# Optimization experiments

Hardware: AMD Instinct MI355X
Metric: run time of the kernel (lower is better)

The kernel has to match this reference:

```python
import jax, jax.numpy as jnp
import numpy as np

DIM = 1024
NUM_HEADS = 8  # only used for the scale; heads are never actually split
SCALE = float((DIM // NUM_HEADS) ** 0.5)


def _attn(x, wq, wk, wv):
    # Single-head full-dim attention, faithful to the source (no head split).
    Q = x @ wq.T  # [B,S,D]
    K = x @ wk.T
    V = x @ wv.T
    scores = jnp.einsum('bqd,bkd->bqk', Q, K) / SCALE  # [B,S,S]
    attn = jax.nn.softmax(scores, axis=-1)
    return jnp.einsum('bqk,bkd->bqd', attn, V)


def setup_inputs() -> dict:
    key = jax.random.key(0)
    ks = jax.random.split(key, 9)
    B, S, D = 4, 2048, DIM
    w = lambda k: jax.random.normal(k, (D, D), dtype=jnp.float32) * 0.02
    return {
        'x': jax.random.normal(ks[0], (B, S, D), dtype=jnp.float32),
        'wq1': w(ks[1]), 'wk1': w(ks[2]), 'wv1': w(ks[3]),
        'fc1_w': w(ks[4]),
        'wq2': w(ks[5]), 'wk2': w(ks[6]), 'wv2': w(ks[7]),
        'fc2_w': w(ks[8]),
    }


def reference(x, wq1, wk1, wv1, fc1_w, wq2, wk2, wv2, fc2_w):
    h = _attn(x, wq1, wk1, wv1)
    h = jax.nn.silu(h)
    h = h @ fc1_w.T
    h = _attn(h, wq2, wk2, wv2)
    h = jax.nn.silu(h)
    h = h @ fc2_w.T
    return jax.nn.softmax(h, axis=-1)
```

## Files before the change

### kernel.cpp

```cpp
#include <hip/hip_runtime.h>
#include <math.h>


typedef __attribute__((ext_vector_type(8))) int i32x8;
typedef __attribute__((ext_vector_type(4))) int i32x4;
typedef __attribute__((ext_vector_type(4))) float f32x4;
typedef unsigned char u8;
typedef unsigned int u32;

#define EPI_F8 1
#define EPI_RV 2
#define EPI_EXP 3
#define EPI_PV 4
#define EPI_EXPF32 5

__device__ __forceinline__ void gload_lds16(const void* g, void* l) {
    __builtin_amdgcn_global_load_lds(
        (const __attribute__((address_space(1))) void*)g,
        (__attribute__((address_space(3))) void*)l, 16, 0, 0);
}

__device__ __forceinline__ u8 cvt_f8(float v) {
    return (u8)(__builtin_amdgcn_cvt_pk_fp8_f32(v, v, 0, false) & 0xFF);
}

__device__ __forceinline__ u32 pack_f8x4(float v0, float v1, float v2, float v3) {
    int p01 = __builtin_amdgcn_cvt_pk_fp8_f32(v0, v1, 0, false);
    int p23 = __builtin_amdgcn_cvt_pk_fp8_f32(v2, v3, 0, false);
    return (u32)(p01 & 0xFFFF) | ((u32)p23 << 16);
}

template <int EPI>
__global__ __launch_bounds__(256) void gemm_fp8(
    const u8* __restrict__ A, const u8* __restrict__ B,
    void* __restrict__ C0, void* __restrict__ C1, void* __restrict__ C2,
    int K, int ldA, int ldB, int ldC,
    long long bsA, long long bsB, long long bsC, float alpha, float beta)
{
    __shared__ u8 sA[128 * 128];
    __shared__ u8 sB[128 * 128];

    const int tid = threadIdx.x;
    const int wave = tid >> 6, lane = tid & 63;
    const int wm = wave >> 1, wn = wave & 1;
    const int m0 = blockIdx.y * 128, n0 = blockIdx.x * 128;
    const long long z = blockIdx.z;

    const u8* pA = A + z * bsA;
    const u8* pB = B + z * bsB;

    int blkid[4], rs_[4], cs16[4];
#pragma unroll
    for (int i = 0; i < 4; i++) {
        blkid[i] = wave * 256 + i * 64 + lane;
        rs_[i] = blkid[i] >> 3;
        cs16[i] = ((blkid[i] & 7) ^ (rs_[i] & 7)) * 16;
    }

    f32x4 acc[4][4] = {};
    const int fr = lane & 15, fc2 = (lane >> 4) * 2;

    for (int k0 = 0; k0 < K; k0 += 128) {
#pragma unroll
        for (int i = 0; i < 4; i++) {
            gload_lds16(pA + (long long)(m0 + rs_[i]) * ldA + k0 + cs16[i],
                        sA + blkid[i] * 16);
            gload_lds16(pB + (long long)(n0 + rs_[i]) * ldB + k0 + cs16[i],
                        sB + blkid[i] * 16);
        }
        __syncthreads();

        i32x8 a[4], b[4];
#pragma unroll
        for (int i = 0; i < 4; i++) {
            const int row = wm * 64 + i * 16 + fr;
            const int sw = row & 7;
            i32x4 lo = *(const i32x4*)(sA + row * 128 + ((fc2 + 0) ^ sw) * 16);
            i32x4 hi = *(const i32x4*)(sA + row * 128 + ((fc2 + 1) ^ sw) * 16);
            a[i] = __builtin_shufflevector(lo, hi, 0, 1, 2, 3, 4, 5, 6, 7);
        }
#pragma unroll
        for (int j = 0; j < 4; j++) {
            const int row = wn * 64 + j * 16 + fr;
            const int sw = row & 7;
            i32x4 lo = *(const i32x4*)(sB + row * 128 + ((fc2 + 0) ^ sw) * 16);
            i32x4 hi = *(const i32x4*)(sB + row * 128 + ((fc2 + 1) ^ sw) * 16);
            b[j] = __builtin_shufflevector(lo, hi, 0, 1, 2, 3, 4, 5, 6, 7);
        }
#pragma unroll
        for (int i = 0; i < 4; i++)
#pragma unroll
            for (int j = 0; j < 4; j++)
                acc[i][j] = __builtin_amdgcn_mfma_scale_f32_16x16x128_f8f6f4(
                    a[i], b[j], acc[i][j], 0 , 0 ,
                    0, 0x7F7F7F7F, 0, 0x7F7F7F7F);
        __syncthreads();
    }

    const int col = lane & 15;
    const int rbase = (lane >> 4) * 4;

    if (EPI == EPI_F8) {
#pragma unroll
        for (int j = 0; j < 4; j++) {
            const int Cq = n0 + wn * 64 + j * 16 + col;
#pragma unroll
            for (int i = 0; i < 4; i++) {
                const int R0 = m0 + wm * 64 + i * 16 + rbase;
                u8* C = (u8*)C0 + z * bsC;
                *(u32*)(C + (long long)Cq * ldC + R0) =
                    pack_f8x4(acc[i][j][0] * alpha, acc[i][j][1] * alpha,
                              acc[i][j][2] * alpha, acc[i][j][3] * alpha);
            }
        }
    }
    (void)beta; (void)C1; (void)C2;
}

template <int EPI>
__global__ __launch_bounds__(512, 2) void gemm256(
    const u8* __restrict__ A, const u8* __restrict__ B,
    void* __restrict__ C0, void* __restrict__ C1, void* __restrict__ C2,
    int K, int ldA, int ldB, int ldC,
    long long bsA, long long bsB, long long bsC, float alpha, float beta)
{
    __shared__ __align__(16) u8 sA[3][128 * 128];
    __shared__ __align__(16) u8 sB[3][256 * 128];

    const int tid = threadIdx.x;
    const int wave = tid >> 6, lane = tid & 63;
    const int wm = wave >> 2, wn = wave & 3;
    const int m0 = blockIdx.y * 128, n0 = blockIdx.x * 256;
    const long long z = blockIdx.z;

    const u8* pA = A + z * bsA;
    const u8* pB = B + z * bsB;

    long long offA[2], offB[4];
    int dstA[2], dstB[4];
#pragma unroll
    for (int l = 0; l < 2; l++) {
        const int id = l * 512 + tid;
        const int r = id >> 3, c = (id & 7) ^ (r & 7);
        offA[l] = (long long)(m0 + r) * ldA + c * 16;
        dstA[l] = id * 16;
    }
#pragma unroll
    for (int l = 0; l < 4; l++) {
        const int id = l * 512 + tid;
        const int r = id >> 3, c = (id & 7) ^ (r & 7);
        offB[l] = (long long)(n0 + r) * ldB + c * 16;
        dstB[l] = id * 16;
    }

    f32x4 acc[4][4] = {};
    const int fr = lane & 15, fc2 = (lane >> 4) * 2;
    const int NT = K >> 7;

    auto STAGE = [&](int t, int buf) {
        const long long kb = (long long)t << 7;
#pragma unroll
        for (int l = 0; l < 2; l++)
            gload_lds16(pA + offA[l] + kb, &sA[buf][dstA[l]]);
#pragma unroll
        for (int l = 0; l < 4; l++)
            gload_lds16(pB + offB[l] + kb, &sB[buf][dstB[l]]);
    };

    auto COMPUTE = [&](int buf) {
        i32x8 a[4], b[4];
#pragma unroll
        for (int i = 0; i < 4; i++) {
            const int row = wm * 64 + i * 16 + fr;
            const int sw = row & 7;
            const u8* p = &sA[buf][row * 128];
            i32x4 lo = *(const i32x4*)(p + ((fc2 + 0) ^ sw) * 16);
            i32x4 hi = *(const i32x4*)(p + ((fc2 + 1) ^ sw) * 16);
            a[i] = __builtin_shufflevector(lo, hi, 0, 1, 2, 3, 4, 5, 6, 7);
        }
#pragma unroll
        for (int j = 0; j < 4; j++) {
            const int row = wn * 64 + j * 16 + fr;
            const int sw = row & 7;
            const u8* p = &sB[buf][row * 128];
            i32x4 lo = *(const i32x4*)(p + ((fc2 + 0) ^ sw) * 16);
            i32x4 hi = *(const i32x4*)(p + ((fc2 + 1) ^ sw) * 16);
            b[j] = __builtin_shufflevector(lo, hi, 0, 1, 2, 3, 4, 5, 6, 7);
        }
        __builtin_amdgcn_s_setprio(1);
#pragma unroll
        for (int i = 0; i < 4; i++)
#pragma unroll
            for (int j = 0; j < 4; j++)
                acc[i][j] = __builtin_amdgcn_mfma_scale_f32_16x16x128_f8f6f4(
                    a[i], b[j], acc[i][j], 0 , 0 ,
                    0, 0x7F7F7F7F, 0, 0x7F7F7F7F);
        __builtin_amdgcn_s_setprio(0);
    };

    STAGE(0, 0);
    STAGE(1, 1);
    asm volatile("s_waitcnt vmcnt(6)" ::: "memory");
    __builtin_amdgcn_s_barrier();
    __builtin_amdgcn_sched_barrier(0);

    int c0 = 0, c1 = 1, c2 = 2;
    for (int t = 0; t < NT - 2; ++t) {
        STAGE(t + 2, c2);
        COMPUTE(c0);
        asm volatile("s_waitcnt vmcnt(6) lgkmcnt(0)" ::: "memory");
        __builtin_amdgcn_s_barrier();
        __builtin_amdgcn_sched_barrier(0);
        const int tmp = c0; c0 = c1; c1 = c2; c2 = tmp;
    }
    COMPUTE(c0);
    asm volatile("s_waitcnt vmcnt(0) lgkmcnt(0)" ::: "memory");
    __builtin_amdgcn_s_barrier();
    __builtin_amdgcn_sched_barrier(0);
    COMPUTE(c1);

    const int col = lane & 15;
    const int rbase = (lane >> 4) * 4;

    if (EPI == EPI_EXP) {
        u8* P = (u8*)C0 + z * bsC;
        float* rsum = (float*)C1 + z * 2048;
#pragma unroll
        for (int j = 0; j < 4; j++) {
            const int Cq = n0 + wn * 64 + j * 16 + col;
            float part = 0.f;
#pragma unroll
            for (int i = 0; i < 4; i++) {
                const int R0 = m0 + wm * 64 + i * 16 + rbase;
                float e0 = __expf(acc[i][j][0] * alpha);
                float e1 = __expf(acc[i][j][1] * alpha);
                float e2 = __expf(acc[i][j][2] * alpha);
                float e3 = __expf(acc[i][j][3] * alpha);
                part += (e0 + e1) + (e2 + e3);
                *(u32*)(P + (long long)Cq * ldC + R0) =
                    pack_f8x4(e0 * 0.0625f, e1 * 0.0625f,
                              e2 * 0.0625f, e3 * 0.0625f);
            }
            part += __shfl_xor(part, 16);
            part += __shfl_xor(part, 32);
            if (lane < 16) atomicAdd(&rsum[Cq], part);
        }
        return;
    }

    if (EPI == EPI_EXPF32) {
        float* Cw = (float*)C0;
        float* rsum = (float*)C1;
#pragma unroll
        for (int j = 0; j < 4; j++) {
            const int Cq = n0 + wn * 64 + j * 16 + col;
            float part = 0.f;
#pragma unroll
            for (int i = 0; i < 4; i++) {
                const int R0 = m0 + wm * 64 + i * 16 + rbase;
                float4 e;
                e.x = __expf(acc[i][j][0] * alpha);
                e.y = __expf(acc[i][j][1] * alpha);
                e.z = __expf(acc[i][j][2] * alpha);
                e.w = __expf(acc[i][j][3] * alpha);
                part += (e.x + e.y) + (e.z + e.w);
                *(float4*)(Cw + (long long)Cq * ldC + R0) = e;
            }
            part += __shfl_xor(part, 16);
            part += __shfl_xor(part, 32);
            if (lane < 16) atomicAdd(&rsum[Cq], part);
        }
        return;
    }

#pragma unroll
    for (int j = 0; j < 4; j++) {
        const int Cq = n0 + wn * 64 + j * 16 + col;
        float inv;
        if (EPI == EPI_PV) {
            const float* rsum = (const float*)C1 + z * 2048;
            inv = alpha / rsum[Cq];
        }
#pragma unroll
        for (int i = 0; i < 4; i++) {
            const int R0 = m0 + wm * 64 + i * 16 + rbase;
            if (EPI == EPI_F8) {
                u8* C = (u8*)C0 + z * bsC;
                *(u32*)(C + (long long)Cq * ldC + R0) =
                    pack_f8x4(acc[i][j][0] * alpha, acc[i][j][1] * alpha,
                              acc[i][j][2] * alpha, acc[i][j][3] * alpha);
            } else if (EPI == EPI_PV) {
                u8* C = (u8*)C0 + z * bsC;
                float v[4];
#pragma unroll
                for (int r = 0; r < 4; r++) {
                    float t = acc[i][j][r] * inv;
                    v[r] = (t / (1.f + __expf(-t))) * beta;
                }
                *(u32*)(C + (long long)Cq * ldC + R0) =
                    pack_f8x4(v[0], v[1], v[2], v[3]);
            } else {
                const int seg = R0 >> 10;
                const int db = R0 & 1023;
                if (seg == 1) {
                    const int bb = Cq >> 11, tt = Cq & 2047;
                    u8* VTp = (u8*)C2;
#pragma unroll
                    for (int r = 0; r < 4; r++)
                        VTp[(long long)bb * (1024LL * 2048) +
                            (long long)(db + r) * 2048 + tt] =
                            cvt_f8(acc[i][j][r] * beta);
                } else {
                    u8* C = (u8*)C0;
                    *(u32*)(C + (long long)Cq * 1024 + db) =
                        pack_f8x4(acc[i][j][0] * alpha, acc[i][j][1] * alpha,
                                  acc[i][j][2] * alpha, acc[i][j][3] * alpha);
                }
            }
        }
    }
}

__global__ __launch_bounds__(256) void convert_all(
    const float* x, const float* wv1, const float* wv2, const float* fc1,
    const float* fc2, u8* __restrict__ ax, u8* __restrict__ bproj,
    u8* __restrict__ wfc, float* __restrict__ rz)
{
    const int bid = blockIdx.x;
    if (bid < 24) {
        float4 zero = {0.f, 0.f, 0.f, 0.f};
        *(float4*)(rz + ((long long)bid * 256 + threadIdx.x) * 4) = zero;
    }
    const float* src;
    u8* dst;
    float scale;
    long long i;
    if (bid < 8192) {
        src = x; dst = ax; scale = 8.f;
        i = ((long long)bid * 256 + threadIdx.x) * 4;
    } else {
        const int idx = bid - 8192;
        const int wi = idx >> 10;
        const float* srcs[4] = {wv1, wv2, fc1, fc2};
        u8* dsts[4] = {bproj + (1 << 20), bproj + 3 * (1 << 20),
                       wfc, wfc + (1 << 20)};
        src = srcs[wi]; dst = dsts[wi]; scale = 256.f;
        i = (((long long)(idx & 1023)) * 256 + threadIdx.x) * 4;
    }
    float4 v = *(const float4*)(src + i);
    *(u32*)(dst + i) = pack_f8x4(v.x * scale, v.y * scale,
                                 v.z * scale, v.w * scale);
}

__global__ __launch_bounds__(256) void convert_t(
    const float* wq1, const float* wk1, const float* wq2, const float* wk2,
    u8* __restrict__ o)
{
    const float* srcs[4] = {wq1, wk1, wq2, wk2};
    const float* src = srcs[blockIdx.y];
    u8* dst = o + (long long)blockIdx.y * (1 << 20);
    const int q0 = (blockIdx.x & 15) * 64, d0 = (blockIdx.x >> 4) * 64;
    const int qq = (threadIdx.x & 15) * 4, dd = (threadIdx.x >> 4) * 4;
    float4 v[4];
#pragma unroll
    for (int s = 0; s < 4; s++)
        v[s] = *(const float4*)(src + (long long)(q0 + qq + s) * 1024 + d0 + dd);
    const float* vf = (const float*)v;
#pragma unroll
    for (int r = 0; r < 4; r++)
        *(u32*)(dst + (long long)(d0 + dd + r) * 1024 + q0 + qq) =
            pack_f8x4(vf[0 * 4 + r] * 256.f, vf[1 * 4 + r] * 256.f,
                      vf[2 * 4 + r] * 256.f, vf[3 * 4 + r] * 256.f);
}

__global__ __launch_bounds__(256) void normalize_1024(
    const float* __restrict__ e, const float* __restrict__ rsum,
    float* __restrict__ out)
{
    const long long row = blockIdx.x;
    const float inv = 1.0f / rsum[row];
    const float* p = e + row * 1024;
    float* o = out + row * 1024;
    float4 v = *(const float4*)(p + threadIdx.x * 4);
    float4 ov;
    ov.x = v.x * inv; ov.y = v.y * inv; ov.z = v.z * inv; ov.w = v.w * inv;
    *(float4*)(o + threadIdx.x * 4) = ov;
}

extern "C" void kernel_launch(void* const* d_in, const int* in_sizes, int n_in,
                              void* d_out, int out_size, void* d_ws, size_t ws_size,
                              hipStream_t stream)
{
    float* out = (float*)d_out;

    constexpr int Bt = 4, S = 2048, D = 1024;
    constexpr int M = Bt * S;
    const long long MD = (long long)M * D;
    const long long DD = (long long)D * D;
    const long long SD = (long long)S * D;
    const long long SS = (long long)S * S;

    u8* Af = (u8*)d_ws;
    u8* Bproj = Af + MD;
    u8* WqT = Bproj + 2 * 2048 * 1024;
    u8* Wfc = WqT + 4 * DD;
    u8* Rf = Wfc + 2 * DD;
    u8* VT = Rf + MD;
    u8* Pf = VT + MD;
    u8* Hs = Pf + (long long)Bt * SS;
    float* SC = (float*)(Hs + MD);
    float* rsum0 = SC + MD;
    float* rsum1 = rsum0 + M;
    float* rsum2 = rsum1 + M;

    const dim3 blk(256);
    const dim3 blk2(512);

    const float SOFT = 0.08838834764831845f;
    const float a_d1   = 1.f / 64.f;
    const float a_R[2] = {1.f / 512.f, 1.f / 1024.f};
    const float b_V[2] = {1.f / 256.f, 1.f / 64.f};
    const float a_qk[2] = {SOFT / 128.f, SOFT / 65536.f};
    const float a_pv[2] = {2.0f, 1.f / 64.f};
    const float b_pv[2] = {256.f, 65536.f};
    const float a_fc[2] = {256.f / 65536.f, 1.f / 16777216.f};

    convert_all<<<dim3(12288), blk, 0, stream>>>(
        (const float*)d_in[0], (const float*)d_in[3], (const float*)d_in[7],
        (const float*)d_in[4], (const float*)d_in[8], Af, Bproj, Wfc, rsum0);
    convert_t<<<dim3(256, 4), blk, 0, stream>>>(
        (const float*)d_in[1], (const float*)d_in[2], (const float*)d_in[5],
        (const float*)d_in[6], WqT);
    gemm_fp8<EPI_F8><<<dim3(8, 8, 2), blk, 0, stream>>>(
        WqT, WqT + DD, Bproj, nullptr, nullptr, D, D, D, D,
        2 * DD, 2 * DD, (long long)2048 * 1024, a_d1, 0.f);

    const dim3 grv(M / 256, 2048 / 128, 1);
    const dim3 gqk(S / 256, S / 128, Bt);
    const dim3 gpv(S / 256, D / 128, Bt);
    const dim3 gw(M / 256, D / 128, 1);

    for (int layer = 0; layer < 2; layer++) {
        const u8* bp = Bproj + (long long)layer * 2048 * 1024;
        const u8* fc = Wfc + (long long)layer * DD;
        float* rsum = layer ? rsum1 : rsum0;

        gemm256<EPI_RV><<<grv, blk2, 0, stream>>>(
            bp, Af, Rf, nullptr, VT, D, D, D, D, 0, 0, 0,
            a_R[layer], b_V[layer]);
        gemm256<EPI_EXP><<<gqk, blk2, 0, stream>>>(
            Af, Rf, Pf, rsum, nullptr, D, D, D, S, SD, SD, SS,
            a_qk[layer], 0.f);
        gemm256<EPI_PV><<<gpv, blk2, 0, stream>>>(
            VT, Pf, Hs, rsum, nullptr, S, S, S, D,
            (long long)D * S, SS, SD, a_pv[layer], b_pv[layer]);
        if (layer == 0) {
            gemm256<EPI_F8><<<gw, blk2, 0, stream>>>(
                fc, Hs, Af, nullptr, nullptr, D, D, D, D, 0, 0, 0,
                a_fc[0], 0.f);
        } else {
            gemm256<EPI_EXPF32><<<gw, blk2, 0, stream>>>(
                fc, Hs, SC, rsum2, nullptr, D, D, D, D, 0, 0, 0,
                a_fc[1], 0.f);
        }
    }

    normalize_1024<<<dim3(M), blk, 0, stream>>>(SC, rsum2, out);
}
```

Measured before the change: 357.4 us.

## Restructure gemm256 into a two-buffer, four-phase interleaved load/MFMA schedule

The triple-buffered gemm256 main loop is replaced with a double-buffered loop. Each K-step is split into four quadrant phases. Each phase reads only the A/B fragments it needs from LDS, issues part of the next tiles' global-to-LDS loads, and runs four MFMAs under raised priority, with barriers between phases. The goal is to spread LDS reads and global loads across the MFMA work and to cut shared memory use. The cost is many more barriers per iteration and less prefetch depth.

```diff
diff --git a/kernel.cpp b/kernel.cpp
--- a/kernel.cpp
+++ b/kernel.cpp
@@ -29,6 +29,10 @@
     int p23 = __builtin_amdgcn_cvt_pk_fp8_f32(v2, v3, 0, false);
     return (u32)(p01 & 0xFFFF) | ((u32)p23 << 16);
 }
+
+#define MFMA_F8(a, b, c) \
+    __builtin_amdgcn_mfma_scale_f32_16x16x128_f8f6f4( \
+        (a), (b), (c), 0, 0, 0, 0x7F7F7F7F, 0, 0x7F7F7F7F)
 
 template <int EPI>
 __global__ __launch_bounds__(256) void gemm_fp8(
@@ -91,9 +95,7 @@
         for (int i = 0; i < 4; i++)
 #pragma unroll
             for (int j = 0; j < 4; j++)
-                acc[i][j] = __builtin_amdgcn_mfma_scale_f32_16x16x128_f8f6f4(
-                    a[i], b[j], acc[i][j], 0 , 0 ,
-                    0, 0x7F7F7F7F, 0, 0x7F7F7F7F);
+                acc[i][j] = MFMA_F8(a[i], b[j], acc[i][j]);
         __syncthreads();
     }
 
@@ -124,8 +126,8 @@
     int K, int ldA, int ldB, int ldC,
     long long bsA, long long bsB, long long bsC, float alpha, float beta)
 {
-    __shared__ __align__(16) u8 sA[3][128 * 128];
-    __shared__ __align__(16) u8 sB[3][256 * 128];
+    __shared__ __align__(16) u8 sA[2][128 * 128];
+    __shared__ __align__(16) u8 sB[2][256 * 128];
 
     const int tid = threadIdx.x;
     const int wave = tid >> 6, lane = tid & 63;
@@ -157,67 +159,101 @@
     const int fr = lane & 15, fc2 = (lane >> 4) * 2;
     const int NT = K >> 7;
 
-    auto STAGE = [&](int t, int buf) {
+    auto SA = [&](int t) {
         const long long kb = (long long)t << 7;
+        u8* base = sA[t & 1];
 #pragma unroll
         for (int l = 0; l < 2; l++)
-            gload_lds16(pA + offA[l] + kb, &sA[buf][dstA[l]]);
-#pragma unroll
-        for (int l = 0; l < 4; l++)
-            gload_lds16(pB + offB[l] + kb, &sB[buf][dstB[l]]);
+            gload_lds16(pA + offA[l] + kb, base + dstA[l]);
     };
-
-    auto COMPUTE = [&](int buf) {
-        i32x8 a[4], b[4];
-#pragma unroll
-        for (int i = 0; i < 4; i++) {
-            const int row = wm * 64 + i * 16 + fr;
-            const int sw = row & 7;
-            const u8* p = &sA[buf][row * 128];
-            i32x4 lo = *(const i32x4*)(p + ((fc2 + 0) ^ sw) * 16);
-            i32x4 hi = *(const i32x4*)(p + ((fc2 + 1) ^ sw) * 16);
-            a[i] = __builtin_shufflevector(lo, hi, 0, 1, 2, 3, 4, 5, 6, 7);
-        }
-#pragma unroll
-        for (int j = 0; j < 4; j++) {
-            const int row = wn * 64 + j * 16 + fr;
-            const int sw = row & 7;
-            const u8* p = &sB[buf][row * 128];
-            i32x4 lo = *(const i32x4*)(p + ((fc2 + 0) ^ sw) * 16);
-            i32x4 hi = *(const i32x4*)(p + ((fc2 + 1) ^ sw) * 16);
-            b[j] = __builtin_shufflevector(lo, hi, 0, 1, 2, 3, 4, 5, 6, 7);
-        }
+    auto SB = [&](int t, int h) {
+        const long long kb = (long long)t << 7;
+        u8* base = sB[t & 1];
+#pragma unroll
+        for (int l = 2 * h; l < 2 * h + 2; l++)
+            gload_lds16(pB + offB[l] + kb, base + dstB[l]);
+    };
+
+    auto RDA = [&](int buf, int i) -> i32x8 {
+        const int row = wm * 64 + i * 16 + fr;
+        const int sw = row & 7;
+        const u8* p = &sA[buf][row * 128];
+        i32x4 lo = *(const i32x4*)(p + ((fc2 + 0) ^ sw) * 16);
+        i32x4 hi = *(const i32x4*)(p + ((fc2 + 1) ^ sw) * 16);
+        return __builtin_shufflevector(lo, hi, 0, 1, 2, 3, 4, 5, 6, 7);
+    };
+    auto RDB = [&](int buf, int j) -> i32x8 {
+        const int row = wn * 64 + j * 16 + fr;
+        const int sw = row & 7;
+        const u8* p = &sB[buf][row * 128];
+        i32x4 lo = *(const i32x4*)(p + ((fc2 + 0) ^ sw) * 16);
+        i32x4 hi = *(const i32x4*)(p + ((fc2 + 1) ^ sw) * 16);
+        return __builtin_shufflevector(lo, hi, 0, 1, 2, 3, 4, 5, 6, 7);
+    };
+
+    SA(0); SB(0, 0); SB(0, 1); SB(1, 0); SB(1, 1);
+    asm volatile("s_waitcnt vmcnt(4)" ::: "memory");
+    __builtin_amdgcn_sched_barrier(0);
+    __builtin_amdgcn_s_barrier();
+
+    for (int t = 0; t < NT; ++t) {
+        const int buf = t & 1;
+        i32x8 a0, a1, a2, a3, b0, b1, b2, b3;
+
+        a0 = RDA(buf, 0); a1 = RDA(buf, 1);
+        b0 = RDB(buf, 0); b1 = RDB(buf, 1);
+        if (t + 1 < NT) SA(t + 1);
+        __builtin_amdgcn_s_barrier();
+        asm volatile("s_waitcnt lgkmcnt(0)" ::: "memory");
+        __builtin_amdgcn_sched_barrier(0);
         __builtin_amdgcn_s_setprio(1);
-#pragma unroll
-        for (int i = 0; i < 4; i++)
-#pragma unroll
-            for (int j = 0; j < 4; j++)
-                acc[i][j] = __builtin_amdgcn_mfma_scale_f32_16x16x128_f8f6f4(
-                    a[i], b[j], acc[i][j], 0 , 0 ,
-                    0, 0x7F7F7F7F, 0, 0x7F7F7F7F);
+        acc[0][0] = MFMA_F8(a0, b0, acc[0][0]);
+        acc[0][1] = MFMA_F8(a0, b1, acc[0][1]);
+        acc[1][0] = MFMA_F8(a1, b0, acc[1][0]);
+        acc[1][1] = MFMA_F8(a1, b1, acc[1][1]);
         __builtin_amdgcn_s_setprio(0);
-    };
-
-    STAGE(0, 0);
-    STAGE(1, 1);
-    asm volatile("s_waitcnt vmcnt(6)" ::: "memory");
-    __builtin_amdgcn_s_barrier();
-    __builtin_amdgcn_sched_barrier(0);
-
-    int c0 = 0, c1 = 1, c2 = 2;
-    for (int t = 0; t < NT - 2; ++t) {
-        STAGE(t + 2, c2);
-        COMPUTE(c0);
-        asm volatile("s_waitcnt vmcnt(6) lgkmcnt(0)" ::: "memory");
-        __builtin_amdgcn_s_barrier();
+        __builtin_amdgcn_s_barrier();
+
+        b2 = RDB(buf, 2); b3 = RDB(buf, 3);
+        __builtin_amdgcn_s_barrier();
+        asm volatile("s_waitcnt lgkmcnt(0)" ::: "memory");
         __builtin_amdgcn_sched_barrier(0);
-        const int tmp = c0; c0 = c1; c1 = c2; c2 = tmp;
-    }
-    COMPUTE(c0);
-    asm volatile("s_waitcnt vmcnt(0) lgkmcnt(0)" ::: "memory");
-    __builtin_amdgcn_s_barrier();
-    __builtin_amdgcn_sched_barrier(0);
-    COMPUTE(c1);
+        __builtin_amdgcn_s_setprio(1);
+        acc[0][2] = MFMA_F8(a0, b2, acc[0][2]);
+        acc[0][3] = MFMA_F8(a0, b3, acc[0][3]);
+        acc[1][2] = MFMA_F8(a1, b2, acc[1][2]);
+        acc[1][3] = MFMA_F8(a1, b3, acc[1][3]);
+        __builtin_amdgcn_s_setprio(0);
+        __builtin_amdgcn_s_barrier();
+
+        a2 = RDA(buf, 2); a3 = RDA(buf, 3);
+        if (t + 2 < NT) SB(t + 2, 0);
+        __builtin_amdgcn_s_barrier();
+        asm volatile("s_waitcnt lgkmcnt(0)" ::: "memory");
+        __builtin_amdgcn_sched_barrier(0);
+        __builtin_amdgcn_s_setprio(1);
+        acc[2][0] = MFMA_F8(a2, b0, acc[2][0]);
+        acc[2][1] = MFMA_F8(a2, b1, acc[2][1]);
+        acc[3][0] = MFMA_F8(a3, b0, acc[3][0]);
+        acc[3][1] = MFMA_F8(a3, b1, acc[3][1]);
+        __builtin_amdgcn_s_setprio(0);
+        __builtin_amdgcn_s_barrier();
+
+        if (t + 2 < NT) SB(t + 2, 1);
+        __builtin_amdgcn_s_barrier();
+        __builtin_amdgcn_s_setprio(1);
+        acc[2][2] = MFMA_F8(a2, b2, acc[2][2]);
+        acc[2][3] = MFMA_F8(a2, b3, acc[2][3]);
+        acc[3][2] = MFMA_F8(a3, b2, acc[3][2]);
+        acc[3][3] = MFMA_F8(a3, b3, acc[3][3]);
+        __builtin_amdgcn_s_setprio(0);
+        if (t + 2 < NT)
+            asm volatile("s_waitcnt vmcnt(4)" ::: "memory");
+        else
+            asm volatile("s_waitcnt vmcnt(0)" ::: "memory");
+        __builtin_amdgcn_sched_barrier(0);
+        __builtin_amdgcn_s_barrier();
+    }
 
     const int col = lane & 15;
     const int rbase = (lane >> 4) * 4;
```

After: 357.6 us. No clear change (+0.0%).

## Replace 128x256 triple-buffered GEMM with 64x256 double-buffered tile kernel

Applied to the files above, without the earlier changes.

The main fp8 GEMM drops its block tile from 128x256 to 64x256. Each of the 8 waves now computes a 64x32 slice instead of a 64x64 quadrant, and the 3-stage pipeline with manual waitcnt and barriers becomes a simple 2-stage double buffer using __syncthreads. Launch bounds move to 4 blocks per CU and grids double in the M dimension. This aims at more occupancy and less LDS per block, but it halves MFMA work per loaded B tile, lowers arithmetic intensity, and drops the priority and scheduling hints.

```diff
diff --git a/kernel.cpp b/kernel.cpp
--- a/kernel.cpp
+++ b/kernel.cpp
@@ -29,6 +29,10 @@
     int p23 = __builtin_amdgcn_cvt_pk_fp8_f32(v2, v3, 0, false);
     return (u32)(p01 & 0xFFFF) | ((u32)p23 << 16);
 }
+
+#define MFMA_F8(a, b, c) \
+    __builtin_amdgcn_mfma_scale_f32_16x16x128_f8f6f4( \
+        (a), (b), (c), 0, 0, 0, 0x7F7F7F7F, 0, 0x7F7F7F7F)
 
 template <int EPI>
 __global__ __launch_bounds__(256) void gemm_fp8(
@@ -91,9 +95,7 @@
         for (int i = 0; i < 4; i++)
 #pragma unroll
             for (int j = 0; j < 4; j++)
-                acc[i][j] = __builtin_amdgcn_mfma_scale_f32_16x16x128_f8f6f4(
-                    a[i], b[j], acc[i][j], 0 , 0 ,
-                    0, 0x7F7F7F7F, 0, 0x7F7F7F7F);
+                acc[i][j] = MFMA_F8(a[i], b[j], acc[i][j]);
         __syncthreads();
     }
 
@@ -118,33 +120,29 @@
 }
 
 template <int EPI>
-__global__ __launch_bounds__(512, 2) void gemm256(
+__global__ __launch_bounds__(512, 4) void gemm64(
     const u8* __restrict__ A, const u8* __restrict__ B,
     void* __restrict__ C0, void* __restrict__ C1, void* __restrict__ C2,
     int K, int ldA, int ldB, int ldC,
     long long bsA, long long bsB, long long bsC, float alpha, float beta)
 {
-    __shared__ __align__(16) u8 sA[3][128 * 128];
-    __shared__ __align__(16) u8 sB[3][256 * 128];
+    __shared__ __align__(16) u8 sA[2][64 * 128];
+    __shared__ __align__(16) u8 sB[2][256 * 128];
 
     const int tid = threadIdx.x;
     const int wave = tid >> 6, lane = tid & 63;
-    const int wm = wave >> 2, wn = wave & 3;
-    const int m0 = blockIdx.y * 128, n0 = blockIdx.x * 256;
+    const int m0 = blockIdx.y * 64, n0 = blockIdx.x * 256;
     const long long z = blockIdx.z;
 
     const u8* pA = A + z * bsA;
     const u8* pB = B + z * bsB;
 
-    long long offA[2], offB[4];
-    int dstA[2], dstB[4];
-#pragma unroll
-    for (int l = 0; l < 2; l++) {
-        const int id = l * 512 + tid;
-        const int r = id >> 3, c = (id & 7) ^ (r & 7);
-        offA[l] = (long long)(m0 + r) * ldA + c * 16;
-        dstA[l] = id * 16;
-    }
+    const int rA = tid >> 3;
+    const long long offA = (long long)(m0 + rA) * ldA +
+                           (((tid & 7) ^ (rA & 7)) * 16);
+    const int dstA = tid * 16;
+    long long offB[4];
+    int dstB[4];
 #pragma unroll
     for (int l = 0; l < 4; l++) {
         const int id = l * 512 + tid;
@@ -153,25 +151,30 @@
         dstB[l] = id * 16;
     }
 
-    f32x4 acc[4][4] = {};
+    f32x4 acc[4][2] = {};
     const int fr = lane & 15, fc2 = (lane >> 4) * 2;
     const int NT = K >> 7;
 
-    auto STAGE = [&](int t, int buf) {
+    auto STAGE = [&](int t) {
         const long long kb = (long long)t << 7;
-#pragma unroll
-        for (int l = 0; l < 2; l++)
-            gload_lds16(pA + offA[l] + kb, &sA[buf][dstA[l]]);
+        const int buf = t & 1;
+        gload_lds16(pA + offA + kb, &sA[buf][dstA]);
 #pragma unroll
         for (int l = 0; l < 4; l++)
             gload_lds16(pB + offB[l] + kb, &sB[buf][dstB[l]]);
     };
 
-    auto COMPUTE = [&](int buf) {
-        i32x8 a[4], b[4];
+    STAGE(0);
+    __syncthreads();
+
+    for (int t = 0; t < NT; ++t) {
+        if (t + 1 < NT) STAGE(t + 1);
+
+        const int buf = t & 1;
+        i32x8 a[4], b[2];
 #pragma unroll
         for (int i = 0; i < 4; i++) {
-            const int row = wm * 64 + i * 16 + fr;
+            const int row = i * 16 + fr;
             const int sw = row & 7;
             const u8* p = &sA[buf][row * 128];
             i32x4 lo = *(const i32x4*)(p + ((fc2 + 0) ^ sw) * 16);
@@ -179,45 +182,22 @@
             a[i] = __builtin_shufflevector(lo, hi, 0, 1, 2, 3, 4, 5, 6, 7);
         }
 #pragma unroll
-        for (int j = 0; j < 4; j++) {
-            const int row = wn * 64 + j * 16 + fr;
+        for (int j = 0; j < 2; j++) {
+            const int row = wave * 32 + j * 16 + fr;
             const int sw = row & 7;
             const u8* p = &sB[buf][row * 128];
             i32x4 lo = *(const i32x4*)(p + ((fc2 + 0) ^ sw) * 16);
             i32x4 hi = *(const i32x4*)(p + ((fc2 + 1) ^ sw) * 16);
             b[j] = __builtin_shufflevector(lo, hi, 0, 1, 2, 3, 4, 5, 6, 7);
         }
-        __builtin_amdgcn_s_setprio(1);
 #pragma unroll
         for (int i = 0; i < 4; i++)
 #pragma unroll
-            for (int j = 0; j < 4; j++)
-                acc[i][j] = __builtin_amdgcn_mfma_scale_f32_16x16x128_f8f6f4(
-                    a[i], b[j], acc[i][j], 0 , 0 ,
-                    0, 0x7F7F7F7F, 0, 0x7F7F7F7F);
-        __builtin_amdgcn_s_setprio(0);
-    };
-
-    STAGE(0, 0);
-    STAGE(1, 1);
-    asm volatile("s_waitcnt vmcnt(6)" ::: "memory");
-    __builtin_amdgcn_s_barrier();
-    __builtin_amdgcn_sched_barrier(0);
-
-    int c0 = 0, c1 = 1, c2 = 2;
-    for (int t = 0; t < NT - 2; ++t) {
-        STAGE(t + 2, c2);
-        COMPUTE(c0);
-        asm volatile("s_waitcnt vmcnt(6) lgkmcnt(0)" ::: "memory");
-        __builtin_amdgcn_s_barrier();
-        __builtin_amdgcn_sched_barrier(0);
-        const int tmp = c0; c0 = c1; c1 = c2; c2 = tmp;
-    }
-    COMPUTE(c0);
-    asm volatile("s_waitcnt vmcnt(0) lgkmcnt(0)" ::: "memory");
-    __builtin_amdgcn_s_barrier();
-    __builtin_amdgcn_sched_barrier(0);
-    COMPUTE(c1);
+            for (int j = 0; j < 2; j++)
+                acc[i][j] = MFMA_F8(a[i], b[j], acc[i][j]);
+
+        __syncthreads();
+    }
 
     const int col = lane & 15;
     const int rbase = (lane >> 4) * 4;
@@ -226,12 +206,12 @@
         u8* P = (u8*)C0 + z * bsC;
         float* rsum = (float*)C1 + z * 2048;
 #pragma unroll
-        for (int j = 0; j < 4; j++) {
-            const int Cq = n0 + wn * 64 + j * 16 + col;
+        for (int j = 0; j < 2; j++) {
+            const int Cq = n0 + wave * 32 + j * 16 + col;
             float part = 0.f;
 #pragma unroll
             for (int i = 0; i < 4; i++) {
-                const int R0 = m0 + wm * 64 + i * 16 + rbase;
+                const int R0 = m0 + i * 16 + rbase;
                 float e0 = __expf(acc[i][j][0] * alpha);
                 float e1 = __expf(acc[i][j][1] * alpha);
                 float e2 = __expf(acc[i][j][2] * alpha);
@@ -252,12 +232,12 @@
         float* Cw = (float*)C0;
         float* rsum = (float*)C1;
 #pragma unroll
-        for (int j = 0; j < 4; j++) {
-            const int Cq = n0 + wn * 64 + j * 16 + col;
+        for (int j = 0; j < 2; j++) {
+            const int Cq = n0 + wave * 32 + j * 16 + col;
             float part = 0.f;
 #pragma unroll
             for (int i = 0; i < 4; i++) {
-                const int R0 = m0 + wm * 64 + i * 16 + rbase;
+                const int R0 = m0 + i * 16 + rbase;
                 float4 e;
                 e.x = __expf(acc[i][j][0] * alpha);
                 e.y = __expf(acc[i][j][1] * alpha);
@@ -274,8 +254,8 @@
     }
 
 #pragma unroll
-    for (int j = 0; j < 4; j++) {
-        const int Cq = n0 + wn * 64 + j * 16 + col;
+    for (int j = 0; j < 2; j++) {
+        const int Cq = n0 + wave * 32 + j * 16 + col;
         float inv;
         if (EPI == EPI_PV) {
             const float* rsum = (const float*)C1 + z * 2048;
@@ -283,7 +263,7 @@
         }
 #pragma unroll
         for (int i = 0; i < 4; i++) {
-            const int R0 = m0 + wm * 64 + i * 16 + rbase;
+            const int R0 = m0 + i * 16 + rbase;
             if (EPI == EPI_F8) {
                 u8* C = (u8*)C0 + z * bsC;
                 *(u32*)(C + (long long)Cq * ldC + R0) =
@@ -435,31 +415,31 @@
         WqT, WqT + DD, Bproj, nullptr, nullptr, D, D, D, D,
         2 * DD, 2 * DD, (long long)2048 * 1024, a_d1, 0.f);
 
-    const dim3 grv(M / 256, 2048 / 128, 1);
-    const dim3 gqk(S / 256, S / 128, Bt);
-    const dim3 gpv(S / 256, D / 128, Bt);
-    const dim3 gw(M / 256, D / 128, 1);
+    const dim3 grv(M / 256, 2048 / 64, 1);
+    const dim3 gqk(S / 256, S / 64, Bt);
+    const dim3 gpv(S / 256, D / 64, Bt);
+    const dim3 gw(M / 256, D / 64, 1);
 
     for (int layer = 0; layer < 2; layer++) {
         const u8* bp = Bproj + (long long)layer * 2048 * 1024;
         const u8* fc = Wfc + (long long)layer * DD;
         float* rsum = layer ? rsum1 : rsum0;
 
-        gemm256<EPI_RV><<<grv, blk2, 0, stream>>>(
+        gemm64<EPI_RV><<<grv, blk2, 0, stream>>>(
             bp, Af, Rf, nullptr, VT, D, D, D, D, 0, 0, 0,
             a_R[layer], b_V[layer]);
-        gemm256<EPI_EXP><<<gqk, blk2, 0, stream>>>(
+        gemm64<EPI_EXP><<<gqk, blk2, 0, stream>>>(
             Af, Rf, Pf, rsum, nullptr, D, D, D, S, SD, SD, SS,
             a_qk[layer], 0.f);
-        gemm256<EPI_PV><<<gpv, blk2, 0, stream>>>(
+        gemm64<EPI_PV><<<gpv, blk2, 0, stream>>>(
             VT, Pf, Hs, rsum, nullptr, S, S, S, D,
             (long long)D * S, SS, SD, a_pv[layer], b_pv[layer]);
         if (layer == 0) {
-            gemm256<EPI_F8><<<gw, blk2, 0, stream>>>(
+            gemm64<EPI_F8><<<gw, blk2, 0, stream>>>(
                 fc, Hs, Af, nullptr, nullptr, D, D, D, D, 0, 0, 0,
                 a_fc[0], 0.f);
         } else {
-            gemm256<EPI_EXPF32><<<gw, blk2, 0, stream>>>(
+            gemm64<EPI_EXPF32><<<gw, blk2, 0, stream>>>(
                 fc, Hs, SC, rsum2, nullptr, D, D, D, D, 0, 0, 0,
                 a_fc[1], 0.f);
         }
```

After: 341.8 us. -4.4%, faster.

## Replace triple-buffered GEMM pipeline with single-buffered synchronous main loop

Applied to the files above, without the earlier changes.

Removes the three-stage LDS ring buffer, manual vmcnt waits, sched barriers and priority hints from the 256-wide FP8 GEMM. Each K step now loads one tile, syncs, computes, and syncs again. LDS use drops from 144KB to 48KB per block and the launch-bounds occupancy hint is gone, which may let more blocks share a CU. In exchange, global loads no longer overlap with MFMA work, so latency is exposed on every iteration.

```diff
diff --git a/kernel.cpp b/kernel.cpp
--- a/kernel.cpp
+++ b/kernel.cpp
@@ -29,6 +29,10 @@
     int p23 = __builtin_amdgcn_cvt_pk_fp8_f32(v2, v3, 0, false);
     return (u32)(p01 & 0xFFFF) | ((u32)p23 << 16);
 }
+
+#define MFMA_F8(a, b, c) \
+    __builtin_amdgcn_mfma_scale_f32_16x16x128_f8f6f4( \
+        (a), (b), (c), 0, 0, 0, 0x7F7F7F7F, 0, 0x7F7F7F7F)
 
 template <int EPI>
 __global__ __launch_bounds__(256) void gemm_fp8(
@@ -91,9 +95,7 @@
         for (int i = 0; i < 4; i++)
 #pragma unroll
             for (int j = 0; j < 4; j++)
-                acc[i][j] = __builtin_amdgcn_mfma_scale_f32_16x16x128_f8f6f4(
-                    a[i], b[j], acc[i][j], 0 , 0 ,
-                    0, 0x7F7F7F7F, 0, 0x7F7F7F7F);
+                acc[i][j] = MFMA_F8(a[i], b[j], acc[i][j]);
         __syncthreads();
     }
 
@@ -118,14 +120,14 @@
 }
 
 template <int EPI>
-__global__ __launch_bounds__(512, 2) void gemm256(
+__global__ __launch_bounds__(512) void gemm256s(
     const u8* __restrict__ A, const u8* __restrict__ B,
     void* __restrict__ C0, void* __restrict__ C1, void* __restrict__ C2,
     int K, int ldA, int ldB, int ldC,
     long long bsA, long long bsB, long long bsC, float alpha, float beta)
 {
-    __shared__ __align__(16) u8 sA[3][128 * 128];
-    __shared__ __align__(16) u8 sB[3][256 * 128];
+    __shared__ __align__(16) u8 sA[128 * 128];
+    __shared__ __align__(16) u8 sB[256 * 128];
 
     const int tid = threadIdx.x;
     const int wave = tid >> 6, lane = tid & 63;
@@ -136,8 +138,7 @@
     const u8* pA = A + z * bsA;
     const u8* pB = B + z * bsB;
 
-    long long offA[2], offB[4];
-    int dstA[2], dstB[4];
+    long long offA[2]; int dstA[2];
 #pragma unroll
     for (int l = 0; l < 2; l++) {
         const int id = l * 512 + tid;
@@ -145,6 +146,7 @@
         offA[l] = (long long)(m0 + r) * ldA + c * 16;
         dstA[l] = id * 16;
     }
+    long long offB[4]; int dstB[4];
 #pragma unroll
     for (int l = 0; l < 4; l++) {
         const int id = l * 512 + tid;
@@ -155,25 +157,22 @@
 
     f32x4 acc[4][4] = {};
     const int fr = lane & 15, fc2 = (lane >> 4) * 2;
-    const int NT = K >> 7;
-
-    auto STAGE = [&](int t, int buf) {
-        const long long kb = (long long)t << 7;
+
+    for (int k0 = 0; k0 < K; k0 += 128) {
 #pragma unroll
         for (int l = 0; l < 2; l++)
-            gload_lds16(pA + offA[l] + kb, &sA[buf][dstA[l]]);
+            gload_lds16(pA + offA[l] + k0, sA + dstA[l]);
 #pragma unroll
         for (int l = 0; l < 4; l++)
-            gload_lds16(pB + offB[l] + kb, &sB[buf][dstB[l]]);
-    };
-
-    auto COMPUTE = [&](int buf) {
+            gload_lds16(pB + offB[l] + k0, sB + dstB[l]);
+        __syncthreads();
+
         i32x8 a[4], b[4];
 #pragma unroll
         for (int i = 0; i < 4; i++) {
             const int row = wm * 64 + i * 16 + fr;
             const int sw = row & 7;
-            const u8* p = &sA[buf][row * 128];
+            const u8* p = sA + row * 128;
             i32x4 lo = *(const i32x4*)(p + ((fc2 + 0) ^ sw) * 16);
             i32x4 hi = *(const i32x4*)(p + ((fc2 + 1) ^ sw) * 16);
             a[i] = __builtin_shufflevector(lo, hi, 0, 1, 2, 3, 4, 5, 6, 7);
@@ -182,42 +181,18 @@
         for (int j = 0; j < 4; j++) {
             const int row = wn * 64 + j * 16 + fr;
             const int sw = row & 7;
-            const u8* p = &sB[buf][row * 128];
+            const u8* p = sB + row * 128;
             i32x4 lo = *(const i32x4*)(p + ((fc2 + 0) ^ sw) * 16);
             i32x4 hi = *(const i32x4*)(p + ((fc2 + 1) ^ sw) * 16);
             b[j] = __builtin_shufflevector(lo, hi, 0, 1, 2, 3, 4, 5, 6, 7);
         }
-        __builtin_amdgcn_s_setprio(1);
 #pragma unroll
         for (int i = 0; i < 4; i++)
 #pragma unroll
             for (int j = 0; j < 4; j++)
-                acc[i][j] = __builtin_amdgcn_mfma_scale_f32_16x16x128_f8f6f4(
-                    a[i], b[j], acc[i][j], 0 , 0 ,
-                    0, 0x7F7F7F7F, 0, 0x7F7F7F7F);
-        __builtin_amdgcn_s_setprio(0);
-    };
-
-    STAGE(0, 0);
-    STAGE(1, 1);
-    asm volatile("s_waitcnt vmcnt(6)" ::: "memory");
-    __builtin_amdgcn_s_barrier();
-    __builtin_amdgcn_sched_barrier(0);
-
-    int c0 = 0, c1 = 1, c2 = 2;
-    for (int t = 0; t < NT - 2; ++t) {
-        STAGE(t + 2, c2);
-        COMPUTE(c0);
-        asm volatile("s_waitcnt vmcnt(6) lgkmcnt(0)" ::: "memory");
-        __builtin_amdgcn_s_barrier();
-        __builtin_amdgcn_sched_barrier(0);
-        const int tmp = c0; c0 = c1; c1 = c2; c2 = tmp;
-    }
-    COMPUTE(c0);
-    asm volatile("s_waitcnt vmcnt(0) lgkmcnt(0)" ::: "memory");
-    __builtin_amdgcn_s_barrier();
-    __builtin_amdgcn_sched_barrier(0);
-    COMPUTE(c1);
+                acc[i][j] = MFMA_F8(a[i], b[j], acc[i][j]);
+        __syncthreads();
+    }
 
     const int col = lane & 15;
     const int rbase = (lane >> 4) * 4;
@@ -445,21 +420,21 @@
         const u8* fc = Wfc + (long long)layer * DD;
         float* rsum = layer ? rsum1 : rsum0;
 
-        gemm256<EPI_RV><<<grv, blk2, 0, stream>>>(
+        gemm256s<EPI_RV><<<grv, blk2, 0, stream>>>(
             bp, Af, Rf, nullptr, VT, D, D, D, D, 0, 0, 0,
             a_R[layer], b_V[layer]);
-        gemm256<EPI_EXP><<<gqk, blk2, 0, stream>>>(
+        gemm256s<EPI_EXP><<<gqk, blk2, 0, stream>>>(
             Af, Rf, Pf, rsum, nullptr, D, D, D, S, SD, SD, SS,
             a_qk[layer], 0.f);
-        gemm256<EPI_PV><<<gpv, blk2, 0, stream>>>(
+        gemm256s<EPI_PV><<<gpv, blk2, 0, stream>>>(
             VT, Pf, Hs, rsum, nullptr, S, S, S, D,
             (long long)D * S, SS, SD, a_pv[layer], b_pv[layer]);
         if (layer == 0) {
-            gemm256<EPI_F8><<<gw, blk2, 0, stream>>>(
+            gemm256s<EPI_F8><<<gw, blk2, 0, stream>>>(
                 fc, Hs, Af, nullptr, nullptr, D, D, D, D, 0, 0, 0,
                 a_fc[0], 0.f);
         } else {
-            gemm256<EPI_EXPF32><<<gw, blk2, 0, stream>>>(
+            gemm256s<EPI_EXPF32><<<gw, blk2, 0, stream>>>(
                 fc, Hs, SC, rsum2, nullptr, D, D, D, D, 0, 0, 0,
                 a_fc[1], 0.f);
         }
```

Measured after the change: 373.1 us. 1.04x slower.
